# Optimization experiments

Measured on AMD Instinct MI355X. Metric: run time of the kernel, lower is better.

Reference implementation:

```python
import jax, jax.numpy as jnp
import numpy as np

D_MODEL = 320
N_HEADS = 8
D_HEADS = 40
D_COND = 768
D_ATTN = N_HEADS * D_HEADS  # 320


def setup_inputs() -> dict:
    key = jax.random.key(0)
    ks = jax.random.split(key, 7)
    B, S, SK = 2, 4096, 4096
    x = jax.random.normal(ks[0], (B, S, D_MODEL), dtype=jnp.float32)
    cond = jax.random.normal(ks[1], (B, SK, D_COND), dtype=jnp.float32)
    # Linear weights stored as [in, out]; torch nn.Linear(in, out) has W [out, in],
    # applied as x @ W.T, equivalent to x @ W_here.
    sq = 1.0 / np.sqrt(D_MODEL)
    sc = 1.0 / np.sqrt(D_COND)
    sa = 1.0 / np.sqrt(D_ATTN)
    Wq = jax.random.uniform(ks[2], (D_MODEL, D_ATTN), jnp.float32, -sq, sq)
    Wk = jax.random.uniform(ks[3], (D_COND, D_ATTN), jnp.float32, -sc, sc)
    Wv = jax.random.uniform(ks[4], (D_COND, D_ATTN), jnp.float32, -sc, sc)
    Wo = jax.random.uniform(ks[5], (D_ATTN, D_MODEL), jnp.float32, -sa, sa)
    bo = jax.random.uniform(ks[6], (D_MODEL,), jnp.float32, -sa, sa)
    return {"x": x, "cond": cond, "Wq": Wq, "Wk": Wk, "Wv": Wv, "Wo": Wo, "bo": bo}


def reference(x, cond, Wq, Wk, Wv, Wo, bo):
    B, S, _ = x.shape
    SK = cond.shape[1]
    scale = D_HEADS ** -0.5
    q = (x @ Wq).reshape(B, S, N_HEADS, D_HEADS)      # [B,S,H,Dh]
    k = (cond @ Wk).reshape(B, SK, N_HEADS, D_HEADS)  # [B,SK,H,Dh]
    v = (cond @ Wv).reshape(B, SK, N_HEADS, D_HEADS)
    # materialized O(N^2) scores, as in the source (einsum -> softmax -> einsum)
    attn = jnp.einsum('bihd,bjhd->bhij', q, k) * scale  # [B,H,S,SK]
    attn = jax.nn.softmax(attn, axis=-1)
    out = jnp.einsum('bhij,bjhd->bihd', attn, v)        # [B,S,H,Dh]
    out = out.reshape(B, S, D_ATTN)
    return out @ Wo + bo
```

## Files before the change

### kernel.cpp

```cpp
#include <hip/hip_runtime.h>

typedef __attribute__((ext_vector_type(8))) short s16x8;
typedef __attribute__((ext_vector_type(8))) __bf16 bf16x8;
typedef __attribute__((ext_vector_type(4))) float f32x4;
typedef __attribute__((ext_vector_type(4))) unsigned short u16x4;
typedef __attribute__((ext_vector_type(4))) unsigned int u32x4;

__device__ __forceinline__ f32x4 mfma_bf16(s16x8 a, s16x8 b, f32x4 c) {
  return __builtin_amdgcn_mfma_f32_16x16x32_bf16(
      __builtin_bit_cast(bf16x8, a), __builtin_bit_cast(bf16x8, b), c, 0, 0, 0);
}

__device__ __forceinline__ unsigned short f2bf(float f) {
  unsigned int u = __builtin_bit_cast(unsigned int, f);
  unsigned int r = u + 0x7FFFu + ((u >> 16) & 1u);
  return (unsigned short)(r >> 16);
}

__device__ __forceinline__ unsigned int cvt_pk_bf16(float lo, float hi) {
  unsigned int d;
  asm volatile("v_cvt_pk_bf16_f32 %0, %1, %2" : "=v"(d) : "v"(lo), "v"(hi));
  return d;
}

__global__ __launch_bounds__(256) void convert_all(const float* __restrict__ x,
                                                   const float* __restrict__ cond,
                                                   unsigned short* __restrict__ xb,
                                                   unsigned short* __restrict__ condb) {
  int i = blockIdx.x * 256 + threadIdx.x;
  const float* in;
  unsigned short* out;
  if (i < 655360) {
    in = x; out = xb;
  } else {
    i -= 655360;
    if (i >= 1572864) return;
    in = cond; out = condb;
  }
  f32x4 v = ((const f32x4*)in)[i];
  u16x4 o;
  o[0] = f2bf(v[0]); o[1] = f2bf(v[1]); o[2] = f2bf(v[2]); o[3] = f2bf(v[3]);
  ((u16x4*)out)[i] = o;
}

__global__ void transpose_all(const float* __restrict__ Wq, const float* __restrict__ Wk,
                              const float* __restrict__ Wv, const float* __restrict__ Wo,
                              unsigned short* __restrict__ WtQ, unsigned short* __restrict__ WtK,
                              unsigned short* __restrict__ WtV, unsigned short* __restrict__ WtO) {
  int id = blockIdx.x * 256 + threadIdx.x;
  const float* in;
  unsigned short* out;
  int K;
  if (id < 102400)      { in = Wq; out = WtQ; K = 320; }
  else if (id < 348160) { in = Wk; out = WtK; K = 768; id -= 102400; }
  else if (id < 593920) { in = Wv; out = WtV; K = 768; id -= 348160; }
  else if (id < 696320) { in = Wo; out = WtO; K = 320; id -= 593920; }
  else return;
  int k = id / 320, n = id - k * 320;
  out[(size_t)n * K + k] = f2bf(in[id]);
}

template <int MODE, int K>
__device__ __forceinline__ void gemm_body(
    const unsigned short* __restrict__ A, const unsigned short* __restrict__ Wt,
    void* __restrict__ dstv, const float* __restrict__ bias, float scale) {
  const int tid = threadIdx.x;
  const int l = tid & 63, w = tid >> 6;
  const int wm = w >> 1, wn = w & 1;
  const int lr = l & 15, lg = l >> 4;
  const int row0 = blockIdx.x * 64 + wm * 32;
  const int col0 = blockIdx.y * 64 + wn * 32;

  const unsigned short* Ap = A + (size_t)(row0 + lr) * K + lg * 8;
  const unsigned short* Bp = Wt + (size_t)(col0 + lr) * K + lg * 8;

  f32x4 acc[2][2];
#pragma unroll
  for (int i = 0; i < 2; i++)
#pragma unroll
    for (int j = 0; j < 2; j++) acc[i][j] = f32x4{0.f, 0.f, 0.f, 0.f};

  constexpr int NB = K / 32;
  s16x8 a0[2], a1[2], b0[2], b1[2];
  a0[0] = *(const s16x8*)(Ap);
  a1[0] = *(const s16x8*)(Ap + (size_t)16 * K);
  b0[0] = *(const s16x8*)(Bp);
  b1[0] = *(const s16x8*)(Bp + (size_t)16 * K);

#pragma unroll
  for (int i = 0; i < NB; i++) {
    const int cur = i & 1, nxt = cur ^ 1;
    if (i + 1 < NB) {
      const int k = (i + 1) * 32;
      a0[nxt] = *(const s16x8*)(Ap + k);
      a1[nxt] = *(const s16x8*)(Ap + (size_t)16 * K + k);
      b0[nxt] = *(const s16x8*)(Bp + k);
      b1[nxt] = *(const s16x8*)(Bp + (size_t)16 * K + k);
    }
    acc[0][0] = mfma_bf16(a0[cur], b0[cur], acc[0][0]);
    acc[0][1] = mfma_bf16(a0[cur], b1[cur], acc[0][1]);
    acc[1][0] = mfma_bf16(a1[cur], b0[cur], acc[1][0]);
    acc[1][1] = mfma_bf16(a1[cur], b1[cur], acc[1][1]);
  }

#pragma unroll
  for (int mf = 0; mf < 2; mf++)
#pragma unroll
    for (int nf = 0; nf < 2; nf++)
#pragma unroll
      for (int r = 0; r < 4; r++) {
        int m = row0 + mf * 16 + lg * 4 + r;
        int n = col0 + nf * 16 + lr;
        float v = acc[mf][nf][r];
        if (MODE == 0 || MODE == 1) {
          int b = m >> 12, s = m & 4095;
          int h = n / 40, d = n - h * 40;
          ((unsigned short*)dstv)[((size_t)(b * 8 + h) * 4096 + s) * 64 + d] =
              f2bf(v * scale);
        } else if (MODE == 2) {
          int b = m >> 12, s = m & 4095;
          int h = n / 40, d = n - h * 40;
          int sp = (s & ~63) | (s & 35) | ((s & 12) << 1) | ((s & 16) >> 2);
          ((unsigned short*)dstv)[((size_t)(b * 8 + h) * 48 + d) * 4096 + sp] = f2bf(v);
        } else {
          ((float*)dstv)[(size_t)m * 320 + n] = v + bias[n];
        }
      }
}

__global__ __launch_bounds__(256) void qkv_proj(
    const unsigned short* __restrict__ xb, const unsigned short* __restrict__ condb,
    const unsigned short* __restrict__ WtQ, const unsigned short* __restrict__ WtK,
    const unsigned short* __restrict__ WtV, unsigned short* __restrict__ Qh,
    unsigned short* __restrict__ Kh, unsigned short* __restrict__ Vt, float qscale) {
  if (blockIdx.z == 0)      gemm_body<0, 320>(xb, WtQ, Qh, nullptr, qscale);
  else if (blockIdx.z == 1) gemm_body<1, 768>(condb, WtK, Kh, nullptr, 1.0f);
  else                      gemm_body<2, 768>(condb, WtV, Vt, nullptr, 1.0f);
}

__global__ __launch_bounds__(256) void o_proj(
    const unsigned short* __restrict__ AO, const unsigned short* __restrict__ WtO,
    float* __restrict__ out, const float* __restrict__ bias) {
  gemm_body<3, 320>(AO, WtO, out, bias, 1.0f);
}

__global__ __launch_bounds__(512) void attn_kernel(
    const unsigned short* __restrict__ Qh, const unsigned short* __restrict__ Kh,
    const unsigned short* __restrict__ Vt, unsigned short* __restrict__ AO) {
  __shared__ __align__(16) char kt[2][8192];
  __shared__ __align__(16) char vts[2][6144];

  const int tid = threadIdx.x;
  const int l = tid & 63, w = tid >> 6;
  const int lr = l & 15, lg = l >> 4;
  const int bh = blockIdx.y;
  const int b = bh >> 3, h = bh & 7;
  const int qbase = blockIdx.x * 128;
  const int qrow = qbase + w * 16 + lr;

  const unsigned short* Qp = Qh + ((size_t)bh * 4096 + qbase + w * 16) * 64;
  const unsigned short* Kp = Kh + (size_t)bh * 4096 * 64;
  const unsigned short* Vp = Vt + (size_t)bh * 48 * 4096;

  const int srow = tid >> 3, sch = tid & 7;
  const bool hasv = (tid < 384);
  const int kofs = ((srow * 128 + sch * 16) ^ ((srow & 7) << 4));

  s16x8 q0 = *(const s16x8*)(Qp + lr * 64 + lg * 8);
  s16x8 q1 = *(const s16x8*)(Qp + lr * 64 + 32 + lg * 8);

  f32x4 O[3];
#pragma unroll
  for (int nf = 0; nf < 3; nf++) O[nf] = f32x4{0.f, 0.f, 0.f, 0.f};
  float rm = -1e30f, rl = 0.f;

  s16x8 kreg = *(const s16x8*)(Kp + (size_t)srow * 64 + sch * 8);
  s16x8 vreg;
  if (hasv) vreg = *(const s16x8*)(Vp + (size_t)srow * 4096 + sch * 8);
  *(s16x8*)(kt[0] + kofs) = kreg;
  if (hasv) *(s16x8*)(vts[0] + kofs) = vreg;
  __syncthreads();

  for (int t = 0; t < 64; ++t) {
    const int kb = t * 64;
    const int p = t & 1;
    const char* ktp = kt[p];
    const char* vtp = vts[p];

    if (t + 1 < 64) {
      kreg = *(const s16x8*)(Kp + (size_t)(kb + 64 + srow) * 64 + sch * 8);
      if (hasv) vreg = *(const s16x8*)(Vp + (size_t)srow * 4096 + kb + 64 + sch * 8);
    }

    f32x4 sf[4];
#pragma unroll
    for (int nf = 0; nf < 4; nf++) sf[nf] = f32x4{0.f, 0.f, 0.f, 0.f};
    __builtin_amdgcn_s_setprio(1);
#pragma unroll
    for (int nf = 0; nf < 4; nf++) {
      int krow = nf * 16 + lr;
      s16x8 kf0 = *(const s16x8*)(ktp + ((krow * 128 + lg * 16) ^ ((krow & 7) << 4)));
      s16x8 kf1 = *(const s16x8*)(ktp + ((krow * 128 + 64 + lg * 16) ^ ((krow & 7) << 4)));
      sf[nf] = mfma_bf16(kf0, q0, sf[nf]);
      sf[nf] = mfma_bf16(kf1, q1, sf[nf]);
    }
    __builtin_amdgcn_s_setprio(0);

    float tm = fmaxf(fmaxf(fmaxf(sf[0][0], sf[0][1]), fmaxf(sf[0][2], sf[0][3])),
                     fmaxf(fmaxf(sf[1][0], sf[1][1]), fmaxf(sf[1][2], sf[1][3])));
    tm = fmaxf(tm, fmaxf(fmaxf(fmaxf(sf[2][0], sf[2][1]), fmaxf(sf[2][2], sf[2][3])),
                         fmaxf(fmaxf(sf[3][0], sf[3][1]), fmaxf(sf[3][2], sf[3][3]))));
    tm = fmaxf(tm, __shfl_xor(tm, 16, 64));
    tm = fmaxf(tm, __shfl_xor(tm, 32, 64));
    if (!__all(tm <= rm)) {
      float mn = fmaxf(rm, tm);
      float al = __builtin_amdgcn_exp2f(rm - mn);
      rm = mn;
      rl *= al;
#pragma unroll
      for (int nf = 0; nf < 3; nf++) {
#pragma unroll
        for (int r = 0; r < 4; r++) O[nf][r] *= al;
      }
    }
    float ts = 0.f;
    unsigned int pk[4][2];
#pragma unroll
    for (int nf = 0; nf < 4; nf++) {
      float p0 = __builtin_amdgcn_exp2f(sf[nf][0] - rm);
      float p1 = __builtin_amdgcn_exp2f(sf[nf][1] - rm);
      float p2 = __builtin_amdgcn_exp2f(sf[nf][2] - rm);
      float p3 = __builtin_amdgcn_exp2f(sf[nf][3] - rm);
      ts += (p0 + p1) + (p2 + p3);
      pk[nf][0] = cvt_pk_bf16(p0, p1);
      pk[nf][1] = cvt_pk_bf16(p2, p3);
    }
    ts += __shfl_xor(ts, 16, 64);
    ts += __shfl_xor(ts, 32, 64);
    rl += ts;

    __builtin_amdgcn_s_setprio(1);
#pragma unroll
    for (int c = 0; c < 2; c++) {
      u32x4 bu = {pk[2 * c][0], pk[2 * c][1], pk[2 * c + 1][0], pk[2 * c + 1][1]};
      s16x8 bfrag = __builtin_bit_cast(s16x8, bu);
#pragma unroll
      for (int nf = 0; nf < 3; nf++) {
        int row = nf * 16 + lr;
        s16x8 afrag = *(const s16x8*)(
            vtp + ((row * 128 + c * 64 + lg * 16) ^ ((row & 7) << 4)));
        O[nf] = mfma_bf16(afrag, bfrag, O[nf]);
      }
    }
    __builtin_amdgcn_s_setprio(0);

    if (t + 1 < 64) {
      *(s16x8*)(kt[p ^ 1] + kofs) = kreg;
      if (hasv) *(s16x8*)(vts[p ^ 1] + kofs) = vreg;
      __syncthreads();
    }
  }

  float inv = 1.f / rl;
#pragma unroll
  for (int nf = 0; nf < 3; nf++) {
#pragma unroll
    for (int r = 0; r < 4; r++) {
      int d = nf * 16 + lg * 4 + r;
      if (d < 40) {
        AO[((size_t)(b * 4096 + qrow)) * 320 + h * 40 + d] = f2bf(O[nf][r] * inv);
      }
    }
  }
}

extern "C" void kernel_launch(void* const* d_in, const int* in_sizes, int n_in,
                              void* d_out, int out_size, void* d_ws,
                              size_t ws_size, hipStream_t stream) {
  const float* x    = (const float*)d_in[0];
  const float* cond = (const float*)d_in[1];
  const float* Wq   = (const float*)d_in[2];
  const float* Wk   = (const float*)d_in[3];
  const float* Wv   = (const float*)d_in[4];
  const float* Wo   = (const float*)d_in[5];
  const float* bo   = (const float*)d_in[6];

  char* ws = (char*)d_ws;
  unsigned short* xb    = (unsigned short*)(ws + 0);
  unsigned short* condb = (unsigned short*)(ws + 5242880);
  unsigned short* WtQ   = (unsigned short*)(ws + 17825792);
  unsigned short* WtK   = (unsigned short*)(ws + 18030592);
  unsigned short* WtV   = (unsigned short*)(ws + 18522112);
  unsigned short* WtO   = (unsigned short*)(ws + 19013632);
  unsigned short* AO    = (unsigned short*)(ws + 19218432);
  unsigned short* Qh    = (unsigned short*)(ws + 24461312);
  unsigned short* Kh    = (unsigned short*)(ws + 32849920);
  unsigned short* Vt    = (unsigned short*)(ws + 41238528);

  hipMemsetAsync(Qh, 0, 23068672, stream);

  convert_all<<<dim3(8704), 256, 0, stream>>>(x, cond, xb, condb);
  transpose_all<<<dim3(2720), 256, 0, stream>>>(Wq, Wk, Wv, Wo, WtQ, WtK, WtV, WtO);

  const float qscale = 1.44269504088896f / sqrtf(40.0f);

  qkv_proj<<<dim3(128, 5, 3), 256, 0, stream>>>(xb, condb, WtQ, WtK, WtV, Qh, Kh, Vt,
                                                qscale);
  attn_kernel<<<dim3(32, 16), 512, 0, stream>>>(Qh, Kh, Vt, AO);
  o_proj<<<dim3(128, 5), 256, 0, stream>>>(AO, WtO, (float*)d_out, bo);
}
```

Baseline: 274.5 us.

## Process two query tiles per wave in attention and deepen GEMM prefetch

The attention kernel now has each wave handle 32 query rows as two 16-row tiles. Each K and V fragment read from LDS is reused for two MFMA chains, and the grid is halved to 16x16 blocks. This reduces LDS traffic and K/V global loads per query and gives more independent MFMAs to overlap with softmax. The cost is higher register pressure and only 256 blocks, which may underfill the GPU's CUs. The GEMM body also moves from double to triple register prefetch of its operands.

```diff
diff --git a/kernel.cpp b/kernel.cpp
--- a/kernel.cpp
+++ b/kernel.cpp
@@ -81,21 +81,27 @@
     for (int j = 0; j < 2; j++) acc[i][j] = f32x4{0.f, 0.f, 0.f, 0.f};
 
   constexpr int NB = K / 32;
-  s16x8 a0[2], a1[2], b0[2], b1[2];
-  a0[0] = *(const s16x8*)(Ap);
-  a1[0] = *(const s16x8*)(Ap + (size_t)16 * K);
-  b0[0] = *(const s16x8*)(Bp);
-  b1[0] = *(const s16x8*)(Bp + (size_t)16 * K);
+  constexpr int D = 3;
+  s16x8 a0[D], a1[D], b0[D], b1[D];
+#pragma unroll
+  for (int i = 0; i < D - 1; i++) {
+    const int k = i * 32;
+    a0[i] = *(const s16x8*)(Ap + k);
+    a1[i] = *(const s16x8*)(Ap + (size_t)16 * K + k);
+    b0[i] = *(const s16x8*)(Bp + k);
+    b1[i] = *(const s16x8*)(Bp + (size_t)16 * K + k);
+  }
 
 #pragma unroll
   for (int i = 0; i < NB; i++) {
-    const int cur = i & 1, nxt = cur ^ 1;
-    if (i + 1 < NB) {
-      const int k = (i + 1) * 32;
-      a0[nxt] = *(const s16x8*)(Ap + k);
-      a1[nxt] = *(const s16x8*)(Ap + (size_t)16 * K + k);
-      b0[nxt] = *(const s16x8*)(Bp + k);
-      b1[nxt] = *(const s16x8*)(Bp + (size_t)16 * K + k);
+    const int cur = i % D;
+    if (i + D - 1 < NB) {
+      const int k = (i + D - 1) * 32;
+      const int sl = (i + D - 1) % D;
+      a0[sl] = *(const s16x8*)(Ap + k);
+      a1[sl] = *(const s16x8*)(Ap + (size_t)16 * K + k);
+      b0[sl] = *(const s16x8*)(Bp + k);
+      b1[sl] = *(const s16x8*)(Bp + (size_t)16 * K + k);
     }
     acc[0][0] = mfma_bf16(a0[cur], b0[cur], acc[0][0]);
     acc[0][1] = mfma_bf16(a0[cur], b1[cur], acc[0][1]);
@@ -155,10 +161,9 @@
   const int lr = l & 15, lg = l >> 4;
   const int bh = blockIdx.y;
   const int b = bh >> 3, h = bh & 7;
-  const int qbase = blockIdx.x * 128;
-  const int qrow = qbase + w * 16 + lr;
-
-  const unsigned short* Qp = Qh + ((size_t)bh * 4096 + qbase + w * 16) * 64;
+  const int qbase = blockIdx.x * 256;
+
+  const unsigned short* Qp = Qh + ((size_t)bh * 4096 + qbase + w * 32) * 64;
   const unsigned short* Kp = Kh + (size_t)bh * 4096 * 64;
   const unsigned short* Vp = Vt + (size_t)bh * 48 * 4096;
 
@@ -166,13 +171,18 @@
   const bool hasv = (tid < 384);
   const int kofs = ((srow * 128 + sch * 16) ^ ((srow & 7) << 4));
 
-  s16x8 q0 = *(const s16x8*)(Qp + lr * 64 + lg * 8);
-  s16x8 q1 = *(const s16x8*)(Qp + lr * 64 + 32 + lg * 8);
-
-  f32x4 O[3];
-#pragma unroll
-  for (int nf = 0; nf < 3; nf++) O[nf] = f32x4{0.f, 0.f, 0.f, 0.f};
-  float rm = -1e30f, rl = 0.f;
+  s16x8 qa0 = *(const s16x8*)(Qp + lr * 64 + lg * 8);
+  s16x8 qa1 = *(const s16x8*)(Qp + lr * 64 + 32 + lg * 8);
+  s16x8 qb0 = *(const s16x8*)(Qp + (16 + lr) * 64 + lg * 8);
+  s16x8 qb1 = *(const s16x8*)(Qp + (16 + lr) * 64 + 32 + lg * 8);
+
+  f32x4 Oa[3], Ob[3];
+#pragma unroll
+  for (int nf = 0; nf < 3; nf++) {
+    Oa[nf] = f32x4{0.f, 0.f, 0.f, 0.f};
+    Ob[nf] = f32x4{0.f, 0.f, 0.f, 0.f};
+  }
+  float rma = -1e30f, rla = 0.f, rmb = -1e30f, rlb = 0.f;
 
   s16x8 kreg = *(const s16x8*)(Kp + (size_t)srow * 64 + sch * 8);
   s16x8 vreg;
@@ -192,64 +202,105 @@
       if (hasv) vreg = *(const s16x8*)(Vp + (size_t)srow * 4096 + kb + 64 + sch * 8);
     }
 
-    f32x4 sf[4];
-#pragma unroll
-    for (int nf = 0; nf < 4; nf++) sf[nf] = f32x4{0.f, 0.f, 0.f, 0.f};
+    f32x4 sfa[4], sfb[4];
+#pragma unroll
+    for (int nf = 0; nf < 4; nf++) {
+      sfa[nf] = f32x4{0.f, 0.f, 0.f, 0.f};
+      sfb[nf] = f32x4{0.f, 0.f, 0.f, 0.f};
+    }
     __builtin_amdgcn_s_setprio(1);
 #pragma unroll
     for (int nf = 0; nf < 4; nf++) {
       int krow = nf * 16 + lr;
       s16x8 kf0 = *(const s16x8*)(ktp + ((krow * 128 + lg * 16) ^ ((krow & 7) << 4)));
       s16x8 kf1 = *(const s16x8*)(ktp + ((krow * 128 + 64 + lg * 16) ^ ((krow & 7) << 4)));
-      sf[nf] = mfma_bf16(kf0, q0, sf[nf]);
-      sf[nf] = mfma_bf16(kf1, q1, sf[nf]);
+      sfa[nf] = mfma_bf16(kf0, qa0, sfa[nf]);
+      sfa[nf] = mfma_bf16(kf1, qa1, sfa[nf]);
+      sfb[nf] = mfma_bf16(kf0, qb0, sfb[nf]);
+      sfb[nf] = mfma_bf16(kf1, qb1, sfb[nf]);
     }
     __builtin_amdgcn_s_setprio(0);
 
-    float tm = fmaxf(fmaxf(fmaxf(sf[0][0], sf[0][1]), fmaxf(sf[0][2], sf[0][3])),
-                     fmaxf(fmaxf(sf[1][0], sf[1][1]), fmaxf(sf[1][2], sf[1][3])));
-    tm = fmaxf(tm, fmaxf(fmaxf(fmaxf(sf[2][0], sf[2][1]), fmaxf(sf[2][2], sf[2][3])),
-                         fmaxf(fmaxf(sf[3][0], sf[3][1]), fmaxf(sf[3][2], sf[3][3]))));
-    tm = fmaxf(tm, __shfl_xor(tm, 16, 64));
-    tm = fmaxf(tm, __shfl_xor(tm, 32, 64));
-    if (!__all(tm <= rm)) {
-      float mn = fmaxf(rm, tm);
-      float al = __builtin_amdgcn_exp2f(rm - mn);
-      rm = mn;
-      rl *= al;
-#pragma unroll
-      for (int nf = 0; nf < 3; nf++) {
-#pragma unroll
-        for (int r = 0; r < 4; r++) O[nf][r] *= al;
-      }
-    }
-    float ts = 0.f;
-    unsigned int pk[4][2];
-#pragma unroll
-    for (int nf = 0; nf < 4; nf++) {
-      float p0 = __builtin_amdgcn_exp2f(sf[nf][0] - rm);
-      float p1 = __builtin_amdgcn_exp2f(sf[nf][1] - rm);
-      float p2 = __builtin_amdgcn_exp2f(sf[nf][2] - rm);
-      float p3 = __builtin_amdgcn_exp2f(sf[nf][3] - rm);
-      ts += (p0 + p1) + (p2 + p3);
-      pk[nf][0] = cvt_pk_bf16(p0, p1);
-      pk[nf][1] = cvt_pk_bf16(p2, p3);
-    }
-    ts += __shfl_xor(ts, 16, 64);
-    ts += __shfl_xor(ts, 32, 64);
-    rl += ts;
+    unsigned int pka[4][2], pkb[4][2];
+    {
+      float tm = fmaxf(fmaxf(fmaxf(sfa[0][0], sfa[0][1]), fmaxf(sfa[0][2], sfa[0][3])),
+                       fmaxf(fmaxf(sfa[1][0], sfa[1][1]), fmaxf(sfa[1][2], sfa[1][3])));
+      tm = fmaxf(tm, fmaxf(fmaxf(fmaxf(sfa[2][0], sfa[2][1]), fmaxf(sfa[2][2], sfa[2][3])),
+                           fmaxf(fmaxf(sfa[3][0], sfa[3][1]), fmaxf(sfa[3][2], sfa[3][3]))));
+      tm = fmaxf(tm, __shfl_xor(tm, 16, 64));
+      tm = fmaxf(tm, __shfl_xor(tm, 32, 64));
+      if (!__all(tm <= rma)) {
+        float mn = fmaxf(rma, tm);
+        float al = __builtin_amdgcn_exp2f(rma - mn);
+        rma = mn;
+        rla *= al;
+#pragma unroll
+        for (int nf = 0; nf < 3; nf++)
+#pragma unroll
+          for (int r = 0; r < 4; r++) Oa[nf][r] *= al;
+      }
+      float ts = 0.f;
+#pragma unroll
+      for (int nf = 0; nf < 4; nf++) {
+        float p0 = __builtin_amdgcn_exp2f(sfa[nf][0] - rma);
+        float p1 = __builtin_amdgcn_exp2f(sfa[nf][1] - rma);
+        float p2 = __builtin_amdgcn_exp2f(sfa[nf][2] - rma);
+        float p3 = __builtin_amdgcn_exp2f(sfa[nf][3] - rma);
+        ts += (p0 + p1) + (p2 + p3);
+        pka[nf][0] = cvt_pk_bf16(p0, p1);
+        pka[nf][1] = cvt_pk_bf16(p2, p3);
+      }
+      ts += __shfl_xor(ts, 16, 64);
+      ts += __shfl_xor(ts, 32, 64);
+      rla += ts;
+    }
+    {
+      float tm = fmaxf(fmaxf(fmaxf(sfb[0][0], sfb[0][1]), fmaxf(sfb[0][2], sfb[0][3])),
+                       fmaxf(fmaxf(sfb[1][0], sfb[1][1]), fmaxf(sfb[1][2], sfb[1][3])));
+      tm = fmaxf(tm, fmaxf(fmaxf(fmaxf(sfb[2][0], sfb[2][1]), fmaxf(sfb[2][2], sfb[2][3])),
+                           fmaxf(fmaxf(sfb[3][0], sfb[3][1]), fmaxf(sfb[3][2], sfb[3][3]))));
+      tm = fmaxf(tm, __shfl_xor(tm, 16, 64));
+      tm = fmaxf(tm, __shfl_xor(tm, 32, 64));
+      if (!__all(tm <= rmb)) {
+        float mn = fmaxf(rmb, tm);
+        float al = __builtin_amdgcn_exp2f(rmb - mn);
+        rmb = mn;
+        rlb *= al;
+#pragma unroll
+        for (int nf = 0; nf < 3; nf++)
+#pragma unroll
+          for (int r = 0; r < 4; r++) Ob[nf][r] *= al;
+      }
+      float ts = 0.f;
+#pragma unroll
+      for (int nf = 0; nf < 4; nf++) {
+        float p0 = __builtin_amdgcn_exp2f(sfb[nf][0] - rmb);
+        float p1 = __builtin_amdgcn_exp2f(sfb[nf][1] - rmb);
+        float p2 = __builtin_amdgcn_exp2f(sfb[nf][2] - rmb);
+        float p3 = __builtin_amdgcn_exp2f(sfb[nf][3] - rmb);
+        ts += (p0 + p1) + (p2 + p3);
+        pkb[nf][0] = cvt_pk_bf16(p0, p1);
+        pkb[nf][1] = cvt_pk_bf16(p2, p3);
+      }
+      ts += __shfl_xor(ts, 16, 64);
+      ts += __shfl_xor(ts, 32, 64);
+      rlb += ts;
+    }
 
     __builtin_amdgcn_s_setprio(1);
 #pragma unroll
     for (int c = 0; c < 2; c++) {
-      u32x4 bu = {pk[2 * c][0], pk[2 * c][1], pk[2 * c + 1][0], pk[2 * c + 1][1]};
-      s16x8 bfrag = __builtin_bit_cast(s16x8, bu);
+      u32x4 bua = {pka[2 * c][0], pka[2 * c][1], pka[2 * c + 1][0], pka[2 * c + 1][1]};
+      u32x4 bub = {pkb[2 * c][0], pkb[2 * c][1], pkb[2 * c + 1][0], pkb[2 * c + 1][1]};
+      s16x8 bfa = __builtin_bit_cast(s16x8, bua);
+      s16x8 bfb = __builtin_bit_cast(s16x8, bub);
 #pragma unroll
       for (int nf = 0; nf < 3; nf++) {
         int row = nf * 16 + lr;
         s16x8 afrag = *(const s16x8*)(
             vtp + ((row * 128 + c * 64 + lg * 16) ^ ((row & 7) << 4)));
-        O[nf] = mfma_bf16(afrag, bfrag, O[nf]);
+        Oa[nf] = mfma_bf16(afrag, bfa, Oa[nf]);
+        Ob[nf] = mfma_bf16(afrag, bfb, Ob[nf]);
       }
     }
     __builtin_amdgcn_s_setprio(0);
@@ -261,14 +312,16 @@
     }
   }
 
-  float inv = 1.f / rl;
+  const int qra = qbase + w * 32 + lr;
+  float inva = 1.f / rla, invb = 1.f / rlb;
 #pragma unroll
   for (int nf = 0; nf < 3; nf++) {
 #pragma unroll
     for (int r = 0; r < 4; r++) {
       int d = nf * 16 + lg * 4 + r;
       if (d < 40) {
-        AO[((size_t)(b * 4096 + qrow)) * 320 + h * 40 + d] = f2bf(O[nf][r] * inv);
+        AO[((size_t)(b * 4096 + qra)) * 320 + h * 40 + d] = f2bf(Oa[nf][r] * inva);
+        AO[((size_t)(b * 4096 + qra + 16)) * 320 + h * 40 + d] = f2bf(Ob[nf][r] * invb);
       }
     }
   }
@@ -306,6 +359,6 @@
 
   qkv_proj<<<dim3(128, 5, 3), 256, 0, stream>>>(xb, condb, WtQ, WtK, WtV, Qh, Kh, Vt,
                                                 qscale);
-  attn_kernel<<<dim3(32, 16), 512, 0, stream>>>(Qh, Kh, Vt, AO);
+  attn_kernel<<<dim3(16, 16), 512, 0, stream>>>(Qh, Kh, Vt, AO);
   o_proj<<<dim3(128, 5), 256, 0, stream>>>(AO, WtO, (float*)d_out, bo);
 }
```

After: 287.2 us. +4.6%, slower.
